# Kernel optimization log

Measured on AMD Instinct MI355X. Metric: run time of the kernel, lower is better.

## Reference

```python
import jax, jax.numpy as jnp
import numpy as np

N, D, K = 32768, 128, 16
EPS = 1e-8  # torch cosine_similarity eps


def setup_inputs() -> dict:
    key = jax.random.key(0)
    k1, k2, kW1, kW2, kV = jax.random.split(key, 5)
    # xavier_normal std for [K, fan_in, fan_out]-style tensors (torch treats dim0 as batch? no:
    # xavier_normal_ on a 3D tensor uses fan_in = D*1? torch computes fan from dims 1.. with receptive field.
    # fan_in = size(1)*rf, fan_out = size(0)*rf where rf = prod(shape[2:]).
    def xavier_std(shape):
        rf = int(np.prod(shape[2:])) if len(shape) > 2 else 1
        fan_in = shape[1] * rf
        fan_out = shape[0] * rf
        return float(np.sqrt(2.0 / (fan_in + fan_out)))
    W1 = jax.random.normal(kW1, (K, D, D), jnp.float32) * xavier_std((K, D, D))
    W2 = jax.random.normal(kW2, (K, D, D), jnp.float32) * xavier_std((K, D, D))
    V = jax.random.normal(kV, (K, 2 * D, 1), jnp.float32) * xavier_std((K, 2 * D, 1))
    b = jnp.zeros((K,), jnp.float32)
    x_1 = jax.random.normal(k1, (N, D), jnp.float32)
    x_2 = jax.random.normal(k2, (N, D), jnp.float32)
    return {"x_1": x_1, "x_2": x_2, "W1": W1, "W2": W2, "V": V, "b": b}


def reference(x_1, x_2, W1, W2, V, b):
    # Batched version of the per-slice loop: one bmm per side instead of K matmuls.
    x1_t = jnp.einsum('nd,kde->kne', x_1, W1)  # [K, N, D]
    x2_t = jnp.einsum('nd,kde->kne', x_2, W2)  # [K, N, D]
    # torch.cosine_similarity(dim=-1): dot / (clamp(||a||, eps) * clamp(||b||, eps))
    num = jnp.sum(x1_t * x2_t, axis=-1)                      # [K, N]
    n1 = jnp.maximum(jnp.sqrt(jnp.sum(x1_t * x1_t, -1)), EPS)
    n2 = jnp.maximum(jnp.sqrt(jnp.sum(x2_t * x2_t, -1)), EPS)
    part1 = num / (n1 * n2)                                  # [K, N]
    x_cat = jnp.concatenate([x_1, x_2], axis=-1)             # [N, 2D]
    part2 = jnp.einsum('nc,kc->kn', x_cat, V[:, :, 0])       # [K, N]
    fea = part1 + part2 + b[:, None]                         # [K, N]
    return jax.nn.relu(fea.T)                                # [N, K]
```

## Files before the change

kernel.cpp:

```cpp
#include <hip/hip_runtime.h>


typedef __attribute__((ext_vector_type(8))) __bf16 bf16x8;
typedef __attribute__((ext_vector_type(8))) unsigned short us8;
typedef __attribute__((ext_vector_type(4))) float f32x4;

static __device__ __forceinline__ unsigned short f2bf(float f) {
  unsigned u = __float_as_uint(f);
  u += 0x7FFFu + ((u >> 16) & 1u);
  return (unsigned short)(u >> 16);
}

static __device__ __forceinline__ bf16x8 as_bf(us8 u) {
  bf16x8 r;
  __builtin_memcpy(&r, &u, sizeof(r));
  return r;
}

__global__ void ntn_prep(const float* __restrict__ W1, const float* __restrict__ W2,
                         const float* __restrict__ V,
                         unsigned short* __restrict__ wsW, unsigned short* __restrict__ wsV) {
  int t = blockIdx.x * 256 + threadIdx.x;
  if (t < 65536) {
    int u = t & 2047;
    int lane = u & 63, s = (u >> 6) & 3, et2 = (u >> 8) & 3, side = (u >> 10) & 1;
    int cc = t >> 11, h = cc & 1, k = cc >> 1;
    int q = lane >> 4, l15 = lane & 15;
    int et = h * 4 + et2;
    const float* W = side ? W2 : W1;
    const float* src = W + k * 16384 + (s * 32 + q * 8) * 128 + (et * 16 + l15);
    us8 r;
#pragma unroll
    for (int j = 0; j < 8; ++j) r[j] = f2bf(src[j * 128]);
    *(us8*)(wsW + (size_t)t * 8) = r;
  } else if (t < 66048) {
    int u = t - 65536;
    int lane = u & 63, cs = u >> 6;
    int q = lane >> 4, l15 = lane & 15;
    const float* src = V + l15 * 256 + cs * 32 + q * 8;
    us8 r;
#pragma unroll
    for (int j = 0; j < 8; ++j) r[j] = f2bf(src[j]);
    *(us8*)(wsV + (size_t)u * 8) = r;
  }
}

__global__ __launch_bounds__(512, 2) void ntn_main(
    const float* __restrict__ x1, const float* __restrict__ x2,
    const float* __restrict__ b,
    const unsigned short* __restrict__ wsW, const unsigned short* __restrict__ wsV,
    float* __restrict__ out) {
  __shared__ uint4 ldsW[2][2048];

  const int tid = threadIdx.x;
  const int lane = tid & 63, wave = tid >> 6;
  const int q = lane >> 4, l15 = lane & 15;

  const int bi = blockIdx.x;
  const int xcd = bi & 7, jj = bi >> 3;
  const int rb = xcd * 16 + (jj >> 2);
  const int kq = jj & 3;
  const int rowbase = rb * 256 + wave * 32;

  const f32x4 zero4 = {0.f, 0.f, 0.f, 0.f};

  auto stage = [&](int cc, int slot) {
    const unsigned short* src = wsW + (size_t)cc * 16384 + (size_t)(wave * 256 + lane) * 8;
    uint4* dst = &ldsW[slot][wave * 256];
#pragma unroll
    for (int i = 0; i < 4; ++i)
      __builtin_amdgcn_global_load_lds(
          (__attribute__((address_space(1))) void*)(void*)(src + i * 512),
          (__attribute__((address_space(3))) void*)(dst + i * 64), 16, 0, 0);
  };

  stage(kq * 8, 0);

  bf16x8 xb[2][2][4];
#pragma unroll
  for (int side = 0; side < 2; ++side) {
    const float* xp0 = side ? x2 : x1;
#pragma unroll
    for (int nt = 0; nt < 2; ++nt) {
#pragma unroll
      for (int s = 0; s < 4; ++s) {
        const float* p = xp0 + (size_t)(rowbase + nt * 16 + l15) * 128 + s * 32 + q * 8;
        float4 v0 = *(const float4*)p;
        float4 v1 = *(const float4*)(p + 4);
        us8 uu;
        uu[0] = f2bf(v0.x); uu[1] = f2bf(v0.y); uu[2] = f2bf(v0.z); uu[3] = f2bf(v0.w);
        uu[4] = f2bf(v1.x); uu[5] = f2bf(v1.y); uu[6] = f2bf(v1.z); uu[7] = f2bf(v1.w);
        xb[side][nt][s] = as_bf(uu);
      }
    }
  }

  f32x4 accP[2];
  {
    bf16x8 vf[8];
#pragma unroll
    for (int cs = 0; cs < 8; ++cs)
      vf[cs] = as_bf(*(const us8*)(wsV + (size_t)(cs * 64 + lane) * 8));
    float4 bv = *(const float4*)(b + q * 4);
#pragma unroll
    for (int nt = 0; nt < 2; ++nt) {
      f32x4 a = zero4;
#pragma unroll
      for (int cs = 0; cs < 8; ++cs)
        a = __builtin_amdgcn_mfma_f32_16x16x32_bf16(vf[cs], xb[cs >> 2][nt][cs & 3], a, 0, 0, 0);
      a.x += bv.x; a.y += bv.y; a.z += bv.z; a.w += bv.w;
      accP[nt] = a;
    }
  }

  float nm[2] = {0.f, 0.f}, q1[2] = {0.f, 0.f}, q2[2] = {0.f, 0.f};

  auto compute = [&](int slot) {
#pragma unroll
    for (int et = 0; et < 4; ++et) {
      bf16x8 wa[4], wb[4];
#pragma unroll
      for (int s = 0; s < 4; ++s) {
        wa[s] = as_bf(*(const us8*)&ldsW[slot][et * 256 + s * 64 + lane]);
        wb[s] = as_bf(*(const us8*)&ldsW[slot][1024 + et * 256 + s * 64 + lane]);
      }
#pragma unroll
      for (int nt = 0; nt < 2; ++nt) {
        f32x4 a1 = zero4, a2 = zero4;
#pragma unroll
        for (int s = 0; s < 4; ++s)
          a1 = __builtin_amdgcn_mfma_f32_16x16x32_bf16(wa[s], xb[0][nt][s], a1, 0, 0, 0);
#pragma unroll
        for (int s = 0; s < 4; ++s)
          a2 = __builtin_amdgcn_mfma_f32_16x16x32_bf16(wb[s], xb[1][nt][s], a2, 0, 0, 0);
        nm[nt] += a1.x * a2.x + a1.y * a2.y + a1.z * a2.z + a1.w * a2.w;
        q1[nt] += a1.x * a1.x + a1.y * a1.y + a1.z * a1.z + a1.w * a1.w;
        q2[nt] += a2.x * a2.x + a2.y * a2.y + a2.z * a2.z + a2.w * a2.w;
      }
    }
  };

#pragma unroll 1
  for (int kk = 0; kk < 4; ++kk) {
    const int cbase = kq * 8 + 2 * kk;
    __syncthreads();
    stage(cbase + 1, 1);
    compute(0);
    __syncthreads();
    if (kk < 3) stage(cbase + 2, 0);
    compute(1);

    const int k = kq * 4 + kk;
    const int qo = k >> 2;
    const int r  = k & 3;
#pragma unroll
    for (int nt = 0; nt < 2; ++nt) {
      float n = nm[nt], s1 = q1[nt], s2 = q2[nt];
      n  += __shfl_xor(n, 16);  n  += __shfl_xor(n, 32);
      s1 += __shfl_xor(s1, 16); s1 += __shfl_xor(s1, 32);
      s2 += __shfl_xor(s2, 16); s2 += __shfl_xor(s2, 32);
      float d1 = fmaxf(sqrtf(s1), 1e-8f);
      float d2 = fmaxf(sqrtf(s2), 1e-8f);
      float p1 = n / (d1 * d2);
      float pc = (r == 0) ? accP[nt].x : (r == 1) ? accP[nt].y
               : (r == 2) ? accP[nt].z : accP[nt].w;
      if (q == qo)
        out[(size_t)(rowbase + nt * 16 + l15) * 16 + k] = fmaxf(p1 + pc, 0.f);
      nm[nt] = 0.f; q1[nt] = 0.f; q2[nt] = 0.f;
    }
  }
}

extern "C" void kernel_launch(void* const* d_in, const int* in_sizes, int n_in,
                              void* d_out, int out_size, void* d_ws, size_t ws_size,
                              hipStream_t stream) {
  const float* x1 = (const float*)d_in[0];
  const float* x2 = (const float*)d_in[1];
  const float* W1 = (const float*)d_in[2];
  const float* W2 = (const float*)d_in[3];
  const float* V  = (const float*)d_in[4];
  const float* b  = (const float*)d_in[5];
  float* out = (float*)d_out;
  unsigned short* wsW = (unsigned short*)d_ws;
  unsigned short* wsV = wsW + (size_t)65536 * 8;

  ntn_prep<<<258, 256, 0, stream>>>(W1, W2, V, wsW, wsV);
  ntn_main<<<512, 512, 0, stream>>>(x1, x2, b, wsW, wsV, out);
}
```

Baseline: 124.4 us.

## Stage only W1 weights in LDS, stream W2 fragments from global with prefetch

The kernel now copies only the W1 half of each weight chunk into shared memory. The W2 fragments are read straight from global memory into registers, with the next slice prefetched one step ahead. Blocks shrink to 256 threads over 128 rows, the grid doubles to 1024, and launch bounds drop to (256,1). The cosine accumulators become packed float2 vectors. The aim is to cut LDS capacity and bandwidth pressure and to gain occupancy and register room. The cost is more L2/global traffic for W2, since every wave now re-reads it, and a higher register count.

```diff
diff --git a/kernel.cpp b/kernel.cpp
--- a/kernel.cpp
+++ b/kernel.cpp
@@ -4,6 +4,7 @@
 typedef __attribute__((ext_vector_type(8))) __bf16 bf16x8;
 typedef __attribute__((ext_vector_type(8))) unsigned short us8;
 typedef __attribute__((ext_vector_type(4))) float f32x4;
+typedef __attribute__((ext_vector_type(2))) float f32x2;
 
 static __device__ __forceinline__ unsigned short f2bf(float f) {
   unsigned u = __float_as_uint(f);
@@ -45,12 +46,12 @@
   }
 }
 
-__global__ __launch_bounds__(512, 2) void ntn_main(
+__global__ __launch_bounds__(256, 1) void ntn_main(
     const float* __restrict__ x1, const float* __restrict__ x2,
     const float* __restrict__ b,
     const unsigned short* __restrict__ wsW, const unsigned short* __restrict__ wsV,
     float* __restrict__ out) {
-  __shared__ uint4 ldsW[2][2048];
+  __shared__ uint4 ldsH[2][1024];
 
   const int tid = threadIdx.x;
   const int lane = tid & 63, wave = tid >> 6;
@@ -58,15 +59,15 @@
 
   const int bi = blockIdx.x;
   const int xcd = bi & 7, jj = bi >> 3;
-  const int rb = xcd * 16 + (jj >> 2);
+  const int rb = xcd * 32 + (jj >> 2);
   const int kq = jj & 3;
-  const int rowbase = rb * 256 + wave * 32;
+  const int rowbase = rb * 128 + wave * 32;
 
   const f32x4 zero4 = {0.f, 0.f, 0.f, 0.f};
 
   auto stage = [&](int cc, int slot) {
-    const unsigned short* src = wsW + (size_t)cc * 16384 + (size_t)(wave * 256 + lane) * 8;
-    uint4* dst = &ldsW[slot][wave * 256];
+    const unsigned short* src = wsW + ((size_t)cc * 2048 + wave * 256 + lane) * 8;
+    uint4* dst = &ldsH[slot][wave * 256];
 #pragma unroll
     for (int i = 0; i < 4; ++i)
       __builtin_amdgcn_global_load_lds(
@@ -113,17 +114,29 @@
     }
   }
 
-  float nm[2] = {0.f, 0.f}, q1[2] = {0.f, 0.f}, q2[2] = {0.f, 0.f};
-
-  auto compute = [&](int slot) {
+  f32x2 nmv[2], q1v[2], q2v[2];
+#pragma unroll
+  for (int nt = 0; nt < 2; ++nt) {
+    nmv[nt] = (f32x2){0.f, 0.f}; q1v[nt] = (f32x2){0.f, 0.f}; q2v[nt] = (f32x2){0.f, 0.f};
+  }
+
+  auto compute = [&](int slot, int cc) {
+    const unsigned short* wsrc = wsW + (size_t)cc * 16384 + 8192;
+    bf16x8 wbc[4], wbn[4];
+#pragma unroll
+    for (int s = 0; s < 4; ++s)
+      wbc[s] = as_bf(*(const us8*)(wsrc + (size_t)(s * 64 + lane) * 8));
 #pragma unroll
     for (int et = 0; et < 4; ++et) {
-      bf16x8 wa[4], wb[4];
-#pragma unroll
-      for (int s = 0; s < 4; ++s) {
-        wa[s] = as_bf(*(const us8*)&ldsW[slot][et * 256 + s * 64 + lane]);
-        wb[s] = as_bf(*(const us8*)&ldsW[slot][1024 + et * 256 + s * 64 + lane]);
+      if (et < 3) {
+#pragma unroll
+        for (int s = 0; s < 4; ++s)
+          wbn[s] = as_bf(*(const us8*)(wsrc + (size_t)((et + 1) * 256 + s * 64 + lane) * 8));
       }
+      bf16x8 wa[4];
+#pragma unroll
+      for (int s = 0; s < 4; ++s)
+        wa[s] = as_bf(*(const us8*)&ldsH[slot][et * 256 + s * 64 + lane]);
 #pragma unroll
       for (int nt = 0; nt < 2; ++nt) {
         f32x4 a1 = zero4, a2 = zero4;
@@ -132,11 +145,15 @@
           a1 = __builtin_amdgcn_mfma_f32_16x16x32_bf16(wa[s], xb[0][nt][s], a1, 0, 0, 0);
 #pragma unroll
         for (int s = 0; s < 4; ++s)
-          a2 = __builtin_amdgcn_mfma_f32_16x16x32_bf16(wb[s], xb[1][nt][s], a2, 0, 0, 0);
-        nm[nt] += a1.x * a2.x + a1.y * a2.y + a1.z * a2.z + a1.w * a2.w;
-        q1[nt] += a1.x * a1.x + a1.y * a1.y + a1.z * a1.z + a1.w * a1.w;
-        q2[nt] += a2.x * a2.x + a2.y * a2.y + a2.z * a2.z + a2.w * a2.w;
+          a2 = __builtin_amdgcn_mfma_f32_16x16x32_bf16(wbc[s], xb[1][nt][s], a2, 0, 0, 0);
+        f32x2 a1lo = {a1.x, a1.y}, a1hi = {a1.z, a1.w};
+        f32x2 a2lo = {a2.x, a2.y}, a2hi = {a2.z, a2.w};
+        nmv[nt] += a1lo * a2lo; nmv[nt] += a1hi * a2hi;
+        q1v[nt] += a1lo * a1lo; q1v[nt] += a1hi * a1hi;
+        q2v[nt] += a2lo * a2lo; q2v[nt] += a2hi * a2hi;
       }
+#pragma unroll
+      for (int s = 0; s < 4; ++s) wbc[s] = wbn[s];
     }
   };
 
@@ -145,17 +162,19 @@
     const int cbase = kq * 8 + 2 * kk;
     __syncthreads();
     stage(cbase + 1, 1);
-    compute(0);
+    compute(0, cbase);
     __syncthreads();
     if (kk < 3) stage(cbase + 2, 0);
-    compute(1);
+    compute(1, cbase + 1);
 
     const int k = kq * 4 + kk;
     const int qo = k >> 2;
     const int r  = k & 3;
 #pragma unroll
     for (int nt = 0; nt < 2; ++nt) {
-      float n = nm[nt], s1 = q1[nt], s2 = q2[nt];
+      float n = nmv[nt].x + nmv[nt].y;
+      float s1 = q1v[nt].x + q1v[nt].y;
+      float s2 = q2v[nt].x + q2v[nt].y;
       n  += __shfl_xor(n, 16);  n  += __shfl_xor(n, 32);
       s1 += __shfl_xor(s1, 16); s1 += __shfl_xor(s1, 32);
       s2 += __shfl_xor(s2, 16); s2 += __shfl_xor(s2, 32);
@@ -166,7 +185,7 @@
                : (r == 2) ? accP[nt].z : accP[nt].w;
       if (q == qo)
         out[(size_t)(rowbase + nt * 16 + l15) * 16 + k] = fmaxf(p1 + pc, 0.f);
-      nm[nt] = 0.f; q1[nt] = 0.f; q2[nt] = 0.f;
+      nmv[nt] = (f32x2){0.f, 0.f}; q1v[nt] = (f32x2){0.f, 0.f}; q2v[nt] = (f32x2){0.f, 0.f};
     }
   }
 }
@@ -185,5 +204,5 @@
   unsigned short* wsV = wsW + (size_t)65536 * 8;
 
   ntn_prep<<<258, 256, 0, stream>>>(W1, W2, V, wsW, wsV);
-  ntn_main<<<512, 512, 0, stream>>>(x1, x2, b, wsW, wsV, out);
-}
+  ntn_main<<<1024, 256, 0, stream>>>(x1, x2, b, wsW, wsV, out);
+}
```

Result: slower. 149.3 us (+20.1%).
